# Kernel tuning notes

Measured on AMD Instinct MI355X. Metric: run time of the kernel, lower is better.

The kernel has to match this reference:

```python
import jax, jax.numpy as jnp
import numpy as np

B, L, HID, NH, HD = 1, 2304, 3072, 24, 128
IMG = 2048
MLP = 4 * HID  # 12288
EPS = 1e-6


def _layernorm(x):
    mu = jnp.mean(x, axis=-1, keepdims=True)
    var = jnp.mean(jnp.square(x - mu), axis=-1, keepdims=True)
    return (x - mu) * jax.lax.rsqrt(var + EPS)


def _rmsnorm(x, w):
    ms = jnp.mean(jnp.square(x), axis=-1, keepdims=True)
    return x * jax.lax.rsqrt(ms + EPS) * w


def _rope_interleaved(x, cos, sin):
    # x: [B, S, H, D]; cos/sin: [1, S, 1, D] with pairwise-equal values (mode=1, GPT-J)
    x1 = x[..., 0::2]
    x2 = x[..., 1::2]
    c = cos[..., 0::2]
    s = sin[..., 0::2]
    even = x1 * c - x2 * s
    odd = x1 * s + x2 * c
    return jnp.stack([even, odd], axis=-1).reshape(x.shape)


def setup_inputs() -> dict:
    key = jax.random.key(0)
    ks = jax.random.split(key, 10)
    scale_in = 1.0 / np.sqrt(HID)
    x = jax.random.normal(ks[0], (B, L, HID), jnp.float32)
    vec = jax.random.normal(ks[1], (B, HID), jnp.float32)
    # RoPE tables (interleaved layout: value repeated per pair)
    pos = jnp.arange(IMG, dtype=jnp.float32)
    inv_freq = 1.0 / (10000.0 ** (jnp.arange(HD // 2, dtype=jnp.float32) / (HD // 2)))
    ang = pos[:, None] * inv_freq[None, :]               # [IMG, HD/2]
    freqs_cos = jnp.repeat(jnp.cos(ang), 2, axis=-1).reshape(1, IMG, 1, HD)
    freqs_sin = jnp.repeat(jnp.sin(ang), 2, axis=-1).reshape(1, IMG, 1, HD)
    mod_w = jax.random.normal(ks[2], (HID, 3 * HID), jnp.float32) * scale_in
    mod_b = jnp.zeros((3 * HID,), jnp.float32)
    w1 = jax.random.normal(ks[3], (HID, 3 * HID + MLP), jnp.float32) * scale_in
    b1 = jnp.zeros((3 * HID + MLP,), jnp.float32)
    q_norm_w = jnp.ones((HD,), jnp.float32)
    k_norm_w = jnp.ones((HD,), jnp.float32)
    w2 = jax.random.normal(ks[4], (HID + MLP, HID), jnp.float32) * (1.0 / np.sqrt(HID + MLP))
    b2 = jnp.zeros((HID,), jnp.float32)
    return {
        'x': x, 'vec': vec, 'img_len': IMG,
        'freqs_cos': freqs_cos, 'freqs_sin': freqs_sin,
        'mod_w': mod_w, 'mod_b': mod_b, 'w1': w1, 'b1': b1,
        'q_norm_w': q_norm_w, 'k_norm_w': k_norm_w, 'w2': w2, 'b2': b2,
    }


def reference(x, vec, img_len, freqs_cos, freqs_sin, mod_w, mod_b, w1, b1,
              q_norm_w, k_norm_w, w2, b2):
    # modulation: SiLU(vec) -> Linear -> shift/scale/gate  [B, HID] each
    mod = jax.nn.silu(vec) @ mod_w + mod_b
    shift, scale, gate = jnp.split(mod, 3, axis=-1)
    x_mod = _layernorm(x) * (1.0 + scale[:, None, :]) + shift[:, None, :]

    # fused QKV + MLP projection
    proj = x_mod @ w1 + b1                                  # [B, L, 3*HID + MLP]
    qkv, mlp = proj[..., :3 * HID], proj[..., 3 * HID:]
    q, k, v = [t[:, :, 0] for t in [None]] if False else None, None, None
    qkv = qkv.reshape(B, L, 3, NH, HD)
    q, k, v = qkv[:, :, 0], qkv[:, :, 1], qkv[:, :, 2]      # [B, L, NH, HD]

    q = _rmsnorm(q, q_norm_w)
    k = _rmsnorm(k, k_norm_w)

    # RoPE only on image tokens
    q = jnp.concatenate([_rope_interleaved(q[:, :img_len], freqs_cos, freqs_sin), q[:, img_len:]], axis=1)
    k = jnp.concatenate([_rope_interleaved(k[:, :img_len], freqs_cos, freqs_sin), k[:, img_len:]], axis=1)

    # full (img+txt) bidirectional attention
    attn_scale = 1.0 / np.sqrt(HD)
    scores = jnp.einsum('blhd,bmhd->bhlm', q, k) * attn_scale
    probs = jax.nn.softmax(scores, axis=-1)
    attn = jnp.einsum('bhlm,bmhd->blhd', probs, v).reshape(B, L, NH * HD)

    # output fusion: [attn | gelu_tanh(mlp)] @ w2
    out = jnp.concatenate([attn, jax.nn.gelu(mlp, approximate=True)], axis=-1) @ w2 + b2
    return x + out * gate[:, None, :]
```

## Files before the change

kernel.cpp:

```cpp
#include <hip/hip_runtime.h>

#define L_SEQ 2304
#define HID_D 3072
#define NH_D 24
#define HD_D 128
#define N1_D 21504
#define QKVN 9216
#define K2_D 15360
#define EPS_V 1e-6f
#define ATTN_SC 0.08838834764831843f

typedef __bf16 bf16x8 __attribute__((ext_vector_type(8)));
typedef float f32x4 __attribute__((ext_vector_type(4)));
typedef unsigned int u32x4 __attribute__((ext_vector_type(4)));
typedef unsigned short u16x8 __attribute__((ext_vector_type(8)));
typedef unsigned short u16x4 __attribute__((ext_vector_type(4)));

#define WAITVM(N) asm volatile("s_waitcnt vmcnt(" #N ")" ::: "memory")
#define LGKM0 asm volatile("s_waitcnt lgkmcnt(0)" ::: "memory")
#define SB0 __builtin_amdgcn_sched_barrier(0)

__device__ __forceinline__ unsigned short f2bf(float f) {
  unsigned int u = __builtin_bit_cast(unsigned int, f);
  u += 0x7fffu + ((u >> 16) & 1u);
  return (unsigned short)(u >> 16);
}
__device__ __forceinline__ float bf2f(unsigned short u) {
  return __builtin_bit_cast(float, (unsigned int)u << 16);
}

__device__ __forceinline__ float gelu_f(float x) {
  float u = 0.7978845608028654f * (x + 0.044715f * x * x * x);
  float e = __expf(2.f * u);
  float th = 1.f - 2.f / (e + 1.f);
  return 0.5f * x * (1.f + th);
}

__device__ __forceinline__ void gload16(const void* g, void* l) {
  __builtin_amdgcn_global_load_lds(
      (const __attribute__((address_space(1))) unsigned int*)g,
      (__attribute__((address_space(3))) unsigned int*)l, 16, 0, 0);
}

__global__ __launch_bounds__(256) void mod_partial_kernel(
    const float* __restrict__ vec, const float* __restrict__ mod_w,
    float* __restrict__ partial) {
  __shared__ float s[384];
  const int t = threadIdx.x;
  const int kb = blockIdx.y;
  const int k0 = kb * 384;
  for (int p = t; p < 384; p += 256) {
    float v = vec[k0 + p];
    s[p] = v / (1.f + __expf(-v));
  }
  __syncthreads();
  const int n = blockIdx.x * 256 + t;
  float acc = 0.f;
  const float* wp = mod_w + (size_t)k0 * QKVN + n;
#pragma unroll 4
  for (int j = 0; j < 384; ++j) acc += s[j] * wp[(size_t)j * QKVN];
  partial[kb * QKVN + n] = acc;
}

__global__ __launch_bounds__(256) void mod_reduce_kernel(
    const float* __restrict__ partial, const float* __restrict__ mod_b,
    float* __restrict__ mod) {
  const int n = blockIdx.x * 256 + threadIdx.x;
  float acc = mod_b[n];
#pragma unroll
  for (int i = 0; i < 8; ++i) acc += partial[i * QKVN + n];
  mod[n] = acc;
}

__global__ __launch_bounds__(256) void ln_mod_kernel(
    const float* __restrict__ x, const float* __restrict__ mod,
    unsigned short* __restrict__ xmod) {
  const int row = blockIdx.x;
  const int t = threadIdx.x;
  const float* xr = x + (size_t)row * HID_D;
  float4 v[3];
  float sum = 0.f, sq = 0.f;
#pragma unroll
  for (int p = 0; p < 3; ++p) {
    v[p] = *(const float4*)&xr[p * 1024 + t * 4];
    sum += v[p].x + v[p].y + v[p].z + v[p].w;
    sq += v[p].x * v[p].x + v[p].y * v[p].y + v[p].z * v[p].z + v[p].w * v[p].w;
  }
#pragma unroll
  for (int o = 1; o < 64; o <<= 1) {
    sum += __shfl_xor(sum, o);
    sq += __shfl_xor(sq, o);
  }
  __shared__ float rs[8];
  const int w = t >> 6;
  if ((t & 63) == 0) { rs[w] = sum; rs[4 + w] = sq; }
  __syncthreads();
  sum = rs[0] + rs[1] + rs[2] + rs[3];
  sq = rs[4] + rs[5] + rs[6] + rs[7];
  const float mu = sum * (1.f / HID_D);
  const float var = sq * (1.f / HID_D) - mu * mu;
  const float rstd = rsqrtf(var + EPS_V);
#pragma unroll
  for (int p = 0; p < 3; ++p) {
    const int c = p * 1024 + t * 4;
    float4 sc = *(const float4*)&mod[3072 + c];
    float4 sh = *(const float4*)&mod[c];
    u16x4 o4;
    o4[0] = f2bf((v[p].x - mu) * rstd * (1.f + sc.x) + sh.x);
    o4[1] = f2bf((v[p].y - mu) * rstd * (1.f + sc.y) + sh.y);
    o4[2] = f2bf((v[p].z - mu) * rstd * (1.f + sc.z) + sh.z);
    o4[3] = f2bf((v[p].w - mu) * rstd * (1.f + sc.w) + sh.w);
    *(u16x4*)&xmod[(size_t)row * HID_D + c] = o4;
  }
}

__global__ __launch_bounds__(256) void convert_transpose_kernel(
    const float* __restrict__ src, unsigned short* __restrict__ dst,
    const int K, const int N) {
  __shared__ unsigned short lt[64][72];
  const int t = threadIdx.x;
  const int n0 = blockIdx.x * 64;
  const int k0 = blockIdx.y * 64;
  const int kr = t >> 4;
  const int n4 = (t & 15) * 4;
#pragma unroll
  for (int p = 0; p < 4; ++p) {
    const int k = kr + p * 16;
    float4 v = *(const float4*)&src[(size_t)(k0 + k) * N + n0 + n4];
    lt[n4 + 0][k] = f2bf(v.x);
    lt[n4 + 1][k] = f2bf(v.y);
    lt[n4 + 2][k] = f2bf(v.z);
    lt[n4 + 3][k] = f2bf(v.w);
  }
  __syncthreads();
  const int nr = t >> 2;
  const int kc = (t & 3) * 16;
  u16x8 a = *(const u16x8*)&lt[nr][kc];
  u16x8 b = *(const u16x8*)&lt[nr][kc + 8];
  unsigned short* dp = &dst[(size_t)(n0 + nr) * K + k0 + kc];
  *(u16x8*)dp = a;
  *(u16x8*)(dp + 8) = b;
}

template <int BM>
__device__ __forceinline__ void gemm8_core(
    const unsigned short* __restrict__ A, const int lda,
    const unsigned short* __restrict__ B, const int ldb,
    const int m0, const int n0, const int nit, char* lds, f32x4 (*acc)[4]) {
  constexpr int AREG = (BM == 256) ? 16384 : 8192;
  constexpr int ABUF = 2 * AREG;
  constexpr int BOFF = 2 * ABUF;
  constexpr int BREG = 16384;
  constexpr int BBUF = 32768;
  constexpr int AROWS = (BM == 256) ? 128 : 64;
  constexpr int AI = (BM == 256) ? 2 : 1;
  constexpr int MF = (BM == 256) ? 4 : 2;
  constexpr int QM = (BM == 256) ? 64 : 32;

  const int t = threadIdx.x;
  const int lane = t & 63;
  const int w = t >> 6;
  const int g = lane >> 4;
  const int c = lane & 15;
  const int sr8 = lane >> 3;
  const int scol = ((lane & 7) ^ sr8) * 8;
  const int arg = w >> 2;
  const int brg = (w & 3) >> 1;
  const int bbase = (w & 1) * 64;

  auto stageA = [&](int buf, int rg, int kt) {
#pragma unroll
    for (int i = 0; i < AI; ++i)
      gload16(A + (size_t)(m0 + rg * AROWS + i * 64 + w * 8 + sr8) * lda +
                  kt * 64 + scol,
              lds + buf * ABUF + rg * AREG + i * 8192 + w * 1024);
  };
  auto stageB = [&](int buf, int rg, int kt) {
#pragma unroll
    for (int i = 0; i < 2; ++i)
      gload16(B + (size_t)(n0 + rg * 128 + i * 64 + w * 8 + sr8) * ldb +
                  kt * 64 + scol,
              lds + BOFF + buf * BBUF + rg * BREG + i * 8192 + w * 1024);
  };

  bf16x8 af[2 * MF], bq0[4], bq1[4];
  auto ldA = [&](int buf, int qm) {
    const char* ab = lds + buf * ABUF + arg * AREG;
#pragma unroll
    for (int i = 0; i < MF; ++i) {
      const int lr = qm * QM + i * 16 + c;
#pragma unroll
      for (int kk = 0; kk < 2; ++kk)
        af[i * 2 + kk] =
            *(const bf16x8*)(ab + lr * 128 + (((kk * 4 + g) ^ (c & 7)) << 4));
    }
  };
  auto ldB = [&](int buf, int qn, bf16x8* bq) {
    const char* bb = lds + BOFF + buf * BBUF + brg * BREG;
#pragma unroll
    for (int i = 0; i < 2; ++i) {
      const int lr = bbase + qn * 32 + i * 16 + c;
#pragma unroll
      for (int kk = 0; kk < 2; ++kk)
        bq[i * 2 + kk] =
            *(const bf16x8*)(bb + lr * 128 + (((kk * 4 + g) ^ (c & 7)) << 4));
    }
  };
  auto domf = [&](int qm, int qn, const bf16x8* bq) {
#pragma unroll
    for (int i = 0; i < MF; ++i)
#pragma unroll
      for (int n = 0; n < 2; ++n)
#pragma unroll
        for (int kk = 0; kk < 2; ++kk)
          acc[qm * MF + i][qn * 2 + n] = __builtin_amdgcn_mfma_f32_16x16x32_bf16(
              af[i * 2 + kk], bq[n * 2 + kk], acc[qm * MF + i][qn * 2 + n], 0, 0, 0);
  };
  auto MID = [&] {
    SB0;
    __builtin_amdgcn_s_barrier();
    LGKM0;
    SB0;
    __builtin_amdgcn_s_setprio(1);
  };
  auto END = [&] {
    __builtin_amdgcn_s_setprio(0);
    SB0;
    __builtin_amdgcn_s_barrier();
  };

  stageB(0, 0, 0); stageA(0, 0, 0); stageB(0, 1, 0); stageA(0, 1, 0);
  stageB(1, 0, 1); stageA(1, 0, 1);
  if constexpr (BM == 256) WAITVM(4); else WAITVM(3);
  __builtin_amdgcn_s_barrier();

  for (int j = 0; j < nit; ++j) {
    const int ta = 2 * j;
    const bool nl = (j + 1 < nit);
    ldA(0, 0); ldB(0, 0, bq0);
    stageB(1, 1, ta + 1);
    MID(); domf(0, 0, bq0); END();
    ldB(0, 1, bq1);
    stageA(1, 1, ta + 1);
    MID(); domf(0, 1, bq1); END();
    ldA(0, 1);
    if (nl) stageB(0, 0, ta + 2);
    MID(); domf(1, 1, bq1); END();
    if (nl) stageA(0, 0, ta + 2);
    MID(); domf(1, 0, bq0);
    __builtin_amdgcn_s_setprio(0); SB0;
    if (nl) { if constexpr (BM == 256) WAITVM(4); else WAITVM(3); }
    else WAITVM(0);
    __builtin_amdgcn_s_barrier();
    ldA(1, 0); ldB(1, 0, bq0);
    if (nl) stageB(0, 1, ta + 2);
    MID(); domf(0, 0, bq0); END();
    ldB(1, 1, bq1);
    if (nl) stageA(0, 1, ta + 2);
    MID(); domf(0, 1, bq1); END();
    ldA(1, 1);
    if (nl) stageB(1, 0, ta + 3);
    MID(); domf(1, 1, bq1); END();
    if (nl) stageA(1, 0, ta + 3);
    MID(); domf(1, 0, bq0);
    __builtin_amdgcn_s_setprio(0); SB0;
    if (nl) { if constexpr (BM == 256) WAITVM(4); else WAITVM(3); }
    __builtin_amdgcn_s_barrier();
  }
}

__global__ __launch_bounds__(512, 2) void gemm1_kernel(
    const unsigned short* __restrict__ xmod, const unsigned short* __restrict__ w1t,
    const float* __restrict__ b1, unsigned short* __restrict__ qkv,
    unsigned short* __restrict__ hbuf) {
  __shared__ __align__(16) char smem[131072];
  f32x4 acc[8][4];
  const f32x4 zero = {0.f, 0.f, 0.f, 0.f};
#pragma unroll
  for (int i = 0; i < 8; ++i)
#pragma unroll
    for (int j = 0; j < 4; ++j) acc[i][j] = zero;
  const int orig = blockIdx.x;
  const int xcd = orig & 7;
  const int wgid = (xcd < 4 ? xcd * 95 : 380 + (xcd - 4) * 94) + (orig >> 3);
  const int m0 = (wgid % 9) * 256;
  const int n0 = (wgid / 9) * 256;
  gemm8_core<256>(xmod, HID_D, w1t, HID_D, m0, n0, 24, smem, acc);
  const int lane = threadIdx.x & 63;
  const int g = lane >> 4, c = lane & 15;
  const int w = threadIdx.x >> 6;
  const int wm = (w >> 2) * 128, wn = (w & 3) * 64;
  const bool is_mlp = (n0 >= QKVN);
#pragma unroll
  for (int mf = 0; mf < 8; ++mf)
#pragma unroll
    for (int nf = 0; nf < 4; ++nf)
#pragma unroll
      for (int j = 0; j < 4; ++j) {
        const int row = m0 + wm + mf * 16 + g * 4 + j;
        const int col = n0 + wn + nf * 16 + c;
        const float v = acc[mf][nf][j] + b1[col];
        if (!is_mlp) {
          qkv[(size_t)row * QKVN + col] = f2bf(v);
        } else {
          hbuf[(size_t)row * K2_D + HID_D + (col - QKVN)] = f2bf(gelu_f(v));
        }
      }
}

__global__ __launch_bounds__(512, 2) void gemm2_kernel(
    const unsigned short* __restrict__ hbuf, const unsigned short* __restrict__ w2t,
    const float* __restrict__ b2, const float* __restrict__ x,
    const float* __restrict__ mod, float* __restrict__ out) {
  __shared__ __align__(16) char smem[98304];
  f32x4 acc[4][4];
  const f32x4 zero = {0.f, 0.f, 0.f, 0.f};
#pragma unroll
  for (int i = 0; i < 4; ++i)
#pragma unroll
    for (int j = 0; j < 4; ++j) acc[i][j] = zero;
  const int orig = blockIdx.x;
  const int wgid = (orig & 7) * 27 + (orig >> 3);
  const int m0 = (wgid % 18) * 128;
  const int n0 = (wgid / 18) * 256;
  gemm8_core<128>(hbuf, K2_D, w2t, K2_D, m0, n0, 120, smem, acc);
  const int lane = threadIdx.x & 63;
  const int g = lane >> 4, c = lane & 15;
  const int w = threadIdx.x >> 6;
  const int wm = (w >> 2) * 64, wn = (w & 3) * 64;
#pragma unroll
  for (int mf = 0; mf < 4; ++mf)
#pragma unroll
    for (int nf = 0; nf < 4; ++nf)
#pragma unroll
      for (int j = 0; j < 4; ++j) {
        const int row = m0 + wm + mf * 16 + g * 4 + j;
        const int col = n0 + wn + nf * 16 + c;
        const float v = acc[mf][nf][j] + b2[col];
        out[(size_t)row * HID_D + col] =
            x[(size_t)row * HID_D + col] + v * mod[6144 + col];
      }
}

__global__ __launch_bounds__(256) void qk_norm_rope_kernel(
    const unsigned short* __restrict__ qkv, const float* __restrict__ qw,
    const float* __restrict__ kw, const float* __restrict__ fc,
    const float* __restrict__ fs, const int* __restrict__ img_len_p,
    unsigned short* __restrict__ qr, unsigned short* __restrict__ kr) {
  const int l = blockIdx.x;
  const int t = threadIdx.x;
  const int wv = t >> 6;
  const int lane = t & 63;
  const int img = *img_len_p;
  const bool do_rope = (l < img);
  float cc = 1.f, ss = 0.f;
  if (do_rope) {
    cc = fc[l * HD_D + 2 * lane];
    ss = fs[l * HD_D + 2 * lane];
  }
  const float qw0 = qw[2 * lane], qw1 = qw[2 * lane + 1];
  const float kw0 = kw[2 * lane], kw1 = kw[2 * lane + 1];
#pragma unroll
  for (int hh = 0; hh < 6; ++hh) {
    const int h = hh * 4 + wv;
    {
      unsigned int pq = *(const unsigned int*)&qkv[(size_t)l * QKVN + h * HD_D + 2 * lane];
      float q0 = bf2f((unsigned short)(pq & 0xffff));
      float q1 = bf2f((unsigned short)(pq >> 16));
      float sq = q0 * q0 + q1 * q1;
#pragma unroll
      for (int o = 1; o < 64; o <<= 1) sq += __shfl_xor(sq, o);
      const float r = rsqrtf(sq * (1.f / HD_D) + EPS_V);
      float a = q0 * r * qw0, b = q1 * r * qw1;
      float e = a, od = b;
      if (do_rope) { e = a * cc - b * ss; od = a * ss + b * cc; }
      e *= ATTN_SC; od *= ATTN_SC;
      unsigned int pk = (unsigned)f2bf(e) | ((unsigned)f2bf(od) << 16);
      *(unsigned int*)&qr[((size_t)h * L_SEQ + l) * HD_D + 2 * lane] = pk;
    }
    {
      unsigned int pkk = *(const unsigned int*)&qkv[(size_t)l * QKVN + HID_D + h * HD_D + 2 * lane];
      float k0 = bf2f((unsigned short)(pkk & 0xffff));
      float k1 = bf2f((unsigned short)(pkk >> 16));
      float sq = k0 * k0 + k1 * k1;
#pragma unroll
      for (int o = 1; o < 64; o <<= 1) sq += __shfl_xor(sq, o);
      const float r = rsqrtf(sq * (1.f / HD_D) + EPS_V);
      float a = k0 * r * kw0, b = k1 * r * kw1;
      float e = a, od = b;
      if (do_rope) { e = a * cc - b * ss; od = a * ss + b * cc; }
      unsigned int pk = (unsigned)f2bf(e) | ((unsigned)f2bf(od) << 16);
      *(unsigned int*)&kr[((size_t)h * L_SEQ + l) * HD_D + 2 * lane] = pk;
    }
  }
}

__global__ __launch_bounds__(256) void v_transpose_kernel(
    const unsigned short* __restrict__ qkv, unsigned short* __restrict__ vT) {
  __shared__ unsigned short lv[128 * 64];
  const int h = blockIdx.y;
  const int l0 = blockIdx.x * 64;
  const int t = threadIdx.x;
#pragma unroll
  for (int p = 0; p < 4; ++p) {
    const int idx = p * 256 + t;
    const int l = idx >> 4;
    const int d8 = (idx & 15) * 8;
    u16x8 v = *(const u16x8*)&qkv[(size_t)(l0 + l) * QKVN + 2 * HID_D + h * HD_D + d8];
#pragma unroll
    for (int e = 0; e < 8; ++e) {
      const int d = d8 + e;
      const unsigned sw = (unsigned)(((d >> 2) & 7) << 4);
      *(unsigned short*)((char*)lv + (((unsigned)d * 128 + 2 * l) ^ sw)) = v[e];
    }
  }
  __syncthreads();
  const int d = t >> 1;
  const int half = t & 1;
  const unsigned swr = (unsigned)(((d >> 2) & 7) << 4);
#pragma unroll
  for (int j2 = 0; j2 < 4; ++j2) {
    u32x4 v = *(const u32x4*)((const char*)lv + ((d * 128 + half * 64 + j2 * 16) ^ swr));
    *(u32x4*)&vT[(size_t)(h * HD_D + d) * L_SEQ + l0 + half * 32 + j2 * 8] = v;
  }
}

__global__ __launch_bounds__(512) void attn_kernel(
    const unsigned short* __restrict__ qr, const unsigned short* __restrict__ kr,
    const unsigned short* __restrict__ vT, unsigned short* __restrict__ hbuf) {
  __shared__ unsigned short lds_k[64 * 128];
  __shared__ unsigned short lds_v[128 * 64];
  __shared__ unsigned short lds_p[8 * 16 * 64];
  const int bid = blockIdx.x;
  const int swz = (bid & 7) * 54 + (bid >> 3);
  const int hidx = swz / 18;
  const int l0 = (swz % 18) * 128;
  const int t = threadIdx.x;
  const int lane = t & 63;
  const int w = t >> 6;
  const int g = lane >> 4;
  const int c = lane & 15;

  bf16x8 qa[4];
  {
    const unsigned short* qrow = qr + ((size_t)hidx * L_SEQ + l0 + w * 16 + c) * HD_D;
#pragma unroll
    for (int ks = 0; ks < 4; ++ks)
      qa[ks] = *(const bf16x8*)&qrow[ks * 32 + g * 8];
  }
  f32x4 acc[8];
  const f32x4 zero = {0.f, 0.f, 0.f, 0.f};
#pragma unroll
  for (int i = 0; i < 8; ++i) acc[i] = zero;
  float m_r[4] = {-1e30f, -1e30f, -1e30f, -1e30f};
  float l_r[4] = {0.f, 0.f, 0.f, 0.f};

  for (int kv0 = 0; kv0 < L_SEQ; kv0 += 64) {
    __syncthreads();
#pragma unroll
    for (int p = 0; p < 2; ++p) {
      const int idx = p * 512 + t;
      const int r = idx >> 4, ch = idx & 15;
      u32x4 v = *(const u32x4*)&kr[((size_t)hidx * L_SEQ + kv0 + r) * HD_D + ch * 8];
      *(u32x4*)((char*)lds_k + ((r * 256 + ch * 16) ^ ((r & 7) << 4))) = v;
    }
#pragma unroll
    for (int p = 0; p < 2; ++p) {
      const int idx = p * 512 + t;
      const int d_ = idx >> 3, ch = idx & 7;
      u32x4 v = *(const u32x4*)&vT[(size_t)(hidx * HD_D + d_) * L_SEQ + kv0 + ch * 8];
      *(u32x4*)((char*)lds_v + ((d_ * 128 + ch * 16) ^ ((d_ & 7) << 4))) = v;
    }
    __syncthreads();
    f32x4 s[4];
#pragma unroll
    for (int cf = 0; cf < 4; ++cf) s[cf] = zero;
#pragma unroll
    for (int ks = 0; ks < 4; ++ks) {
      const int kb = (ks * 32 + g * 8) * 2;
#pragma unroll
      for (int cf = 0; cf < 4; ++cf) {
        const int kvr = cf * 16 + c;
        bf16x8 kf = *(const bf16x8*)((const char*)lds_k + ((kvr * 256 + kb) ^ ((kvr & 7) << 4)));
        s[cf] = __builtin_amdgcn_mfma_f32_16x16x32_bf16(qa[ks], kf, s[cf], 0, 0, 0);
      }
    }
    float pv[4][4];
    float alpha[4];
#pragma unroll
    for (int r = 0; r < 4; ++r) {
      float mx = fmaxf(fmaxf(s[0][r], s[1][r]), fmaxf(s[2][r], s[3][r]));
      mx = fmaxf(mx, __shfl_xor(mx, 1));
      mx = fmaxf(mx, __shfl_xor(mx, 2));
      mx = fmaxf(mx, __shfl_xor(mx, 4));
      mx = fmaxf(mx, __shfl_xor(mx, 8));
      const float mnew = fmaxf(m_r[r], mx);
      alpha[r] = __expf(m_r[r] - mnew);
      float rsum = 0.f;
#pragma unroll
      for (int cf = 0; cf < 4; ++cf) {
        const float p_ = __expf(s[cf][r] - mnew);
        pv[cf][r] = p_;
        rsum += p_;
      }
      rsum += __shfl_xor(rsum, 1);
      rsum += __shfl_xor(rsum, 2);
      rsum += __shfl_xor(rsum, 4);
      rsum += __shfl_xor(rsum, 8);
      l_r[r] = l_r[r] * alpha[r] + rsum;
      m_r[r] = mnew;
    }
#pragma unroll
    for (int of = 0; of < 8; ++of)
#pragma unroll
      for (int r = 0; r < 4; ++r) acc[of][r] *= alpha[r];
#pragma unroll
    for (int cf = 0; cf < 4; ++cf)
#pragma unroll
      for (int r = 0; r < 4; ++r) {
        const int row = g * 4 + r;
        const int col = cf * 16 + c;
        *(unsigned short*)((char*)lds_p +
                           ((w * 2048 + row * 128 + col * 2) ^ ((row & 7) << 4))) =
            f2bf(pv[cf][r]);
      }
    asm volatile("s_waitcnt lgkmcnt(0)" ::: "memory");
    __builtin_amdgcn_sched_barrier(0);
#pragma unroll
    for (int ks = 0; ks < 2; ++ks) {
      bf16x8 pa = *(const bf16x8*)((const char*)lds_p +
                                   ((w * 2048 + c * 128 + (ks * 32 + g * 8) * 2) ^
                                    ((c & 7) << 4)));
#pragma unroll
      for (int of = 0; of < 8; ++of) {
        const int dcol = of * 16 + c;
        bf16x8 vb = *(const bf16x8*)((const char*)lds_v +
                                     ((dcol * 128 + (ks * 32 + g * 8) * 2) ^
                                      ((dcol & 7) << 4)));
        acc[of] = __builtin_amdgcn_mfma_f32_16x16x32_bf16(pa, vb, acc[of], 0, 0, 0);
      }
    }
  }
  float rinv[4];
#pragma unroll
  for (int r = 0; r < 4; ++r) rinv[r] = 1.f / l_r[r];
#pragma unroll
  for (int of = 0; of < 8; ++of)
#pragma unroll
    for (int r = 0; r < 4; ++r) {
      const int row = l0 + w * 16 + g * 4 + r;
      const int col = hidx * HD_D + of * 16 + c;
      hbuf[(size_t)row * K2_D + col] = f2bf(acc[of][r] * rinv[r]);
    }
}

extern "C" void kernel_launch(void* const* d_in, const int* in_sizes, int n_in,
                              void* d_out, int out_size, void* d_ws, size_t ws_size,
                              hipStream_t stream) {
  (void)in_sizes; (void)n_in; (void)out_size; (void)ws_size;
  const float* x = (const float*)d_in[0];
  const float* vec = (const float*)d_in[1];
  const int* img_len = (const int*)d_in[2];
  const float* fc = (const float*)d_in[3];
  const float* fs = (const float*)d_in[4];
  const float* mod_w = (const float*)d_in[5];
  const float* mod_b = (const float*)d_in[6];
  const float* w1 = (const float*)d_in[7];
  const float* b1 = (const float*)d_in[8];
  const float* qw = (const float*)d_in[9];
  const float* kw = (const float*)d_in[10];
  const float* w2 = (const float*)d_in[11];
  const float* b2 = (const float*)d_in[12];
  float* out = (float*)d_out;

  char* wsb = (char*)d_ws;
  float* mod = (float*)(wsb + 0);
  float* partial = (float*)(wsb + 36864);
  unsigned short* xmod = (unsigned short*)(wsb + 331776);
  unsigned short* qkv = (unsigned short*)(wsb + 14487552);
  unsigned short* hbuf = (unsigned short*)(wsb + 99422208);
  unsigned short* qr = (unsigned short*)(wsb + 170201088);
  unsigned short* kr = (unsigned short*)(wsb + 184356864);
  unsigned short* vT = (unsigned short*)(wsb + 198512640);
  unsigned short* wt = (unsigned short*)(wsb + 212668416);

  mod_partial_kernel<<<dim3(36, 8), 256, 0, stream>>>(vec, mod_w, partial);
  mod_reduce_kernel<<<36, 256, 0, stream>>>(partial, mod_b, mod);
  ln_mod_kernel<<<2304, 256, 0, stream>>>(x, mod, xmod);
  convert_transpose_kernel<<<dim3(N1_D / 64, HID_D / 64), 256, 0, stream>>>(
      w1, wt, HID_D, N1_D);
  gemm1_kernel<<<756, 512, 0, stream>>>(xmod, wt, b1, qkv, hbuf);
  convert_transpose_kernel<<<dim3(HID_D / 64, K2_D / 64), 256, 0, stream>>>(
      w2, wt, K2_D, HID_D);
  qk_norm_rope_kernel<<<2304, 256, 0, stream>>>(qkv, qw, kw, fc, fs, img_len, qr, kr);
  v_transpose_kernel<<<dim3(36, 24), 256, 0, stream>>>(qkv, vT);
  attn_kernel<<<432, 512, 0, stream>>>(qr, kr, vT, hbuf);
  gemm2_kernel<<<216, 512, 0, stream>>>(hbuf, wt, b2, x, mod, out);
}
```

Measured before the change: 946.1 us.

## Double-buffer attention K/V tiles with direct global-to-LDS loads and smaller blocks

The attention kernel now stages K and V tiles through a two-slot LDS buffer using direct global-to-LDS loads (gload16). The next tile is prefetched while the current one is consumed, so the two __syncthreads per iteration and the register round trip are gone. Blocks shrink from 512 threads covering 128 query rows to 256 threads covering 64 rows, on a 36x24 grid with no block swizzle. This adds LDS per block and doubles K/V global traffic per query row. It also drops the L2-friendly head swizzle, which could reduce cache reuse.

```diff
diff --git a/kernel.cpp b/kernel.cpp
--- a/kernel.cpp
+++ b/kernel.cpp
@@ -425,22 +425,39 @@
   }
 }
 
-__global__ __launch_bounds__(512) void attn_kernel(
+__global__ __launch_bounds__(256) void attn_kernel(
     const unsigned short* __restrict__ qr, const unsigned short* __restrict__ kr,
     const unsigned short* __restrict__ vT, unsigned short* __restrict__ hbuf) {
-  __shared__ unsigned short lds_k[64 * 128];
-  __shared__ unsigned short lds_v[128 * 64];
-  __shared__ unsigned short lds_p[8 * 16 * 64];
-  const int bid = blockIdx.x;
-  const int swz = (bid & 7) * 54 + (bid >> 3);
-  const int hidx = swz / 18;
-  const int l0 = (swz % 18) * 128;
+  __shared__ unsigned short lds_k[2][64 * 128];
+  __shared__ unsigned short lds_v[2][128 * 64];
+  __shared__ unsigned short lds_p[4 * 16 * 64];
+  const int hidx = blockIdx.y;
+  const int l0 = blockIdx.x * 64;
   const int t = threadIdx.x;
   const int lane = t & 63;
   const int w = t >> 6;
   const int g = lane >> 4;
   const int c = lane & 15;
 
+  const int krow = w * 16 + (lane >> 4);
+  const int kcol_e = ((lane & 15) ^ ((lane >> 4) & 7)) * 8;
+  const int kcol_o = ((lane & 15) ^ (((lane >> 4) + 4) & 7)) * 8;
+  const int vrow = w * 32 + (lane >> 3);
+  const int vcol = ((lane & 7) ^ ((lane >> 3) & 7)) * 8;
+
+  auto stage = [&](int buf, int kv0) {
+#pragma unroll
+    for (int i = 0; i < 4; ++i) {
+      const int col = (i & 1) ? kcol_o : kcol_e;
+      gload16(kr + ((size_t)hidx * L_SEQ + kv0 + krow + i * 4) * HD_D + col,
+              (char*)lds_k + buf * 16384 + w * 4096 + i * 1024);
+    }
+#pragma unroll
+    for (int i = 0; i < 4; ++i)
+      gload16(vT + ((size_t)(hidx * HD_D) + vrow + i * 8) * L_SEQ + kv0 + vcol,
+              (char*)lds_v + buf * 16384 + w * 4096 + i * 1024);
+  };
+
   bf16x8 qa[4];
   {
     const unsigned short* qrow = qr + ((size_t)hidx * L_SEQ + l0 + w * 16 + c) * HD_D;
@@ -455,23 +472,16 @@
   float m_r[4] = {-1e30f, -1e30f, -1e30f, -1e30f};
   float l_r[4] = {0.f, 0.f, 0.f, 0.f};
 
+  stage(0, 0);
+  SB0; WAITVM(0);
+  __builtin_amdgcn_s_barrier();
+
+  int cur = 0;
   for (int kv0 = 0; kv0 < L_SEQ; kv0 += 64) {
-    __syncthreads();
-#pragma unroll
-    for (int p = 0; p < 2; ++p) {
-      const int idx = p * 512 + t;
-      const int r = idx >> 4, ch = idx & 15;
-      u32x4 v = *(const u32x4*)&kr[((size_t)hidx * L_SEQ + kv0 + r) * HD_D + ch * 8];
-      *(u32x4*)((char*)lds_k + ((r * 256 + ch * 16) ^ ((r & 7) << 4))) = v;
-    }
-#pragma unroll
-    for (int p = 0; p < 2; ++p) {
-      const int idx = p * 512 + t;
-      const int d_ = idx >> 3, ch = idx & 7;
-      u32x4 v = *(const u32x4*)&vT[(size_t)(hidx * HD_D + d_) * L_SEQ + kv0 + ch * 8];
-      *(u32x4*)((char*)lds_v + ((d_ * 128 + ch * 16) ^ ((d_ & 7) << 4))) = v;
-    }
-    __syncthreads();
+    const bool nl = (kv0 + 64 < L_SEQ);
+    if (nl) stage(cur ^ 1, kv0 + 64);
+    const char* bk = (const char*)lds_k + cur * 16384;
+    const char* bv = (const char*)lds_v + cur * 16384;
     f32x4 s[4];
 #pragma unroll
     for (int cf = 0; cf < 4; ++cf) s[cf] = zero;
@@ -481,7 +491,7 @@
 #pragma unroll
       for (int cf = 0; cf < 4; ++cf) {
         const int kvr = cf * 16 + c;
-        bf16x8 kf = *(const bf16x8*)((const char*)lds_k + ((kvr * 256 + kb) ^ ((kvr & 7) << 4)));
+        bf16x8 kf = *(const bf16x8*)(bk + ((kvr * 256 + kb) ^ ((kvr & 7) << 4)));
         s[cf] = __builtin_amdgcn_mfma_f32_16x16x32_bf16(qa[ks], kf, s[cf], 0, 0, 0);
       }
     }
@@ -524,8 +534,8 @@
                            ((w * 2048 + row * 128 + col * 2) ^ ((row & 7) << 4))) =
             f2bf(pv[cf][r]);
       }
-    asm volatile("s_waitcnt lgkmcnt(0)" ::: "memory");
-    __builtin_amdgcn_sched_barrier(0);
+    LGKM0;
+    SB0;
 #pragma unroll
     for (int ks = 0; ks < 2; ++ks) {
       bf16x8 pa = *(const bf16x8*)((const char*)lds_p +
@@ -534,11 +544,15 @@
 #pragma unroll
       for (int of = 0; of < 8; ++of) {
         const int dcol = of * 16 + c;
-        bf16x8 vb = *(const bf16x8*)((const char*)lds_v +
-                                     ((dcol * 128 + (ks * 32 + g * 8) * 2) ^
-                                      ((dcol & 7) << 4)));
+        bf16x8 vb = *(const bf16x8*)(bv + ((dcol * 128 + (ks * 32 + g * 8) * 2) ^
+                                           ((dcol & 7) << 4)));
         acc[of] = __builtin_amdgcn_mfma_f32_16x16x32_bf16(pa, vb, acc[of], 0, 0, 0);
       }
+    }
+    if (nl) {
+      SB0; WAITVM(0);
+      __builtin_amdgcn_s_barrier();
+      cur ^= 1;
     }
   }
   float rinv[4];
@@ -594,6 +608,6 @@
       w2, wt, K2_D, HID_D);
   qk_norm_rope_kernel<<<2304, 256, 0, stream>>>(qkv, qw, kw, fc, fs, img_len, qr, kr);
   v_transpose_kernel<<<dim3(36, 24), 256, 0, stream>>>(qkv, vT);
-  attn_kernel<<<432, 512, 0, stream>>>(qr, kr, vT, hbuf);
+  attn_kernel<<<dim3(36, 24), 256, 0, stream>>>(qr, kr, vT, hbuf);
   gemm2_kernel<<<216, 512, 0, stream>>>(hbuf, wt, b2, x, mod, out);
 }
```

Result: no change. 957.6 us (+1.2%).
